# Performance work log

Hardware: AMD Instinct MI355X
Metric: run time of the kernel (lower is better)

Reference implementation:

```python
import jax, jax.numpy as jnp
import numpy as np

V_THRESH = 0.3

@jax.custom_vjp
def spike(x):
    return (x > 0).astype(x.dtype)

def _spike_fwd(x):
    return spike(x), x

def _spike_bwd(x, g):
    # rectangular straight-through surrogate gradient (pass grad where |x| < 0.5)
    return (g * (jnp.abs(x) < 0.5).astype(g.dtype),)

spike.defvjp(_spike_fwd, _spike_bwd)


def setup_inputs() -> dict:
    key = jax.random.key(0)
    B, T, H = 128, 2048, 128
    k1, = jax.random.split(key, 1)
    x_seq = jax.random.normal(k1, (B, T, H), dtype=jnp.float32)
    v0 = jnp.zeros((B, H), dtype=jnp.float32)
    z0 = jnp.zeros((B, H), dtype=jnp.float32)
    decay_raw = jnp.zeros((H,), dtype=jnp.float32)  # nn.initializers.constant(0.0)
    return {"x_seq": x_seq, "v0": v0, "z0": z0, "decay_raw": decay_raw}


def reference(x_seq, v0, z0, decay_raw):
    # LIF recurrence: v_t = v_{t-1} * decay * (1 - z_{t-1}) + x_t ; z_t = spike(v_t - v_thresh)
    decay = jax.nn.sigmoid(decay_raw)  # (H,)

    def step(carry, x_t):
        v, z = carry
        v = v * decay * (1.0 - z) + x_t
        z_out = spike(v - V_THRESH)
        return (v, z_out), z_out

    x_tb = jnp.swapaxes(x_seq, 0, 1)  # [T, B, H] for lax.scan over time
    (_, _), spk_tb = jax.lax.scan(step, (v0, z0), x_tb)
    return jnp.swapaxes(spk_tb, 0, 1)  # [B, T, H]
```

## Files before the change

### kernel.cpp

```cpp
#include <hip/hip_runtime.h>
#include <math.h>


constexpr int Bdim = 128;
constexpr int Tdim = 2048;
constexpr int Hdim = 128;
constexpr int HW   = 64;
constexpr int U    = 128;
constexpr int NBUF = 4;
constexpr int NW   = 8;
constexpr int NTILE = Tdim / U;
constexpr float VTH = 0.3f;

typedef const __attribute__((address_space(1))) void* gptr_t;
typedef __attribute__((address_space(3))) void* lptr_t;

__global__ __launch_bounds__(NW * 64) void lif_kernel(
    const float* __restrict__ x,
    const float* __restrict__ v0,
    const float* __restrict__ z0,
    const float* __restrict__ decay_raw,
    float* __restrict__ out)
{
    __shared__ float lds[NBUF][U][HW];

    const int tid  = threadIdx.x;
    const int wave = tid >> 6;
    const int lane = tid & 63;
    const int blk  = blockIdx.x;
    const int b    = blk >> 1;
    const int h0   = (blk & 1) * HW;

    const float* xbase = x   + (size_t)b * Tdim * Hdim + h0;
    float*       obase = out + (size_t)b * Tdim * Hdim + h0;

    const int sub = (lane >> 4) * Hdim + (lane & 15) * 4;

    auto fill = [&](int tile, int buf) {
        const float* g = xbase + (size_t)tile * U * Hdim + sub;
        #pragma unroll
        for (int q = 0; q < 4; ++q) {
            const int jj = wave * 4 + q;
            __builtin_amdgcn_global_load_lds(
                (gptr_t)(const void*)(g + (size_t)(4 * jj) * Hdim),
                (lptr_t)(void*)&lds[buf][4 * jj][0],
                16, 0, 0);
        }
    };

    auto flush = [&](int tile, int buf) {
        #pragma unroll
        for (int q = 0; q < 4; ++q) {
            const int s   = wave * 4 + q;
            const int row = 4 * s + (lane >> 4);
            const int col = (lane & 15) * 4;
            const float4 vv = *(const float4*)&lds[buf][row][col];
            *(float4*)(obase + (size_t)(tile * U + row) * Hdim + col) = vv;
        }
    };

    float decay = 0.f, v = 0.f, z = 0.f;
    if (wave == 0) {
        decay = 1.0f / (1.0f + expf(-decay_raw[h0 + lane]));
        v = v0[b * Hdim + h0 + lane];
        z = z0[b * Hdim + h0 + lane];
    }

    fill(0, 0);
    fill(1, 1);
    __syncthreads();

    for (int k = 0; k < NTILE; ++k) {
        if (k + 2 < NTILE) fill(k + 2, (k + 2) % NBUF);
        if (k >= 1)        flush(k - 1, (k - 1) % NBUF);

        if (wave == 0) {
            const int cb = k % NBUF;
            #pragma unroll 16
            for (int tl = 0; tl < U; ++tl) {
                const float xv = lds[cb][tl][lane];
                const float vd = v * decay;
                v = ((z > 0.5f) ? 0.0f : vd) + xv;
                z = (v > VTH) ? 1.0f : 0.0f;
                lds[cb][tl][lane] = z;
            }
        }
        __syncthreads();
    }
    flush(NTILE - 1, (NTILE - 1) % NBUF);
}

extern "C" void kernel_launch(void* const* d_in, const int* in_sizes, int n_in,
                              void* d_out, int out_size, void* d_ws, size_t ws_size,
                              hipStream_t stream) {
    const float* x         = (const float*)d_in[0];
    const float* v0        = (const float*)d_in[1];
    const float* z0        = (const float*)d_in[2];
    const float* decay_raw = (const float*)d_in[3];
    float* out = (float*)d_out;

    lif_kernel<<<Bdim * Hdim / HW, NW * 64, 0, stream>>>(x, v0, z0, decay_raw, out);
}
```

Before: 242.0 us.

## Specialize waves into compute, loader and storer roles with explicit waitcnt barriers

Moves from 8 waves to 4 per block with fixed roles. Wave 0 runs the recurrence and double-buffers its LDS reads of x in 16-step register batches. Waves 1-2 issue async global-to-LDS loads and wait on vmcnt counters instead of a full drain. Wave 3 flushes finished tiles to global memory. Raw s_barrier and waitcnt asm replace __syncthreads, which removes wasted work on the compute wave. The risk is correctness: the hand-tuned vmcnt thresholds and barrier placement must be right for the 4-buffer ring to be safe.

```diff
diff --git a/kernel.cpp b/kernel.cpp
--- a/kernel.cpp
+++ b/kernel.cpp
@@ -8,14 +8,18 @@
 constexpr int HW   = 64;
 constexpr int U    = 128;
 constexpr int NBUF = 4;
-constexpr int NW   = 8;
 constexpr int NTILE = Tdim / U;
 constexpr float VTH = 0.3f;
 
 typedef const __attribute__((address_space(1))) void* gptr_t;
 typedef __attribute__((address_space(3))) void* lptr_t;
 
-__global__ __launch_bounds__(NW * 64) void lif_kernel(
+#define BAR()     asm volatile("s_barrier" ::: "memory")
+#define WAITV16() asm volatile("s_waitcnt vmcnt(16)" ::: "memory")
+#define WAITV0()  asm volatile("s_waitcnt vmcnt(0)" ::: "memory")
+#define WAITL0()  asm volatile("s_waitcnt lgkmcnt(0)" ::: "memory")
+
+__global__ __launch_bounds__(256) void lif_kernel(
     const float* __restrict__ x,
     const float* __restrict__ v0,
     const float* __restrict__ z0,
@@ -39,8 +43,8 @@
     auto fill = [&](int tile, int buf) {
         const float* g = xbase + (size_t)tile * U * Hdim + sub;
         #pragma unroll
-        for (int q = 0; q < 4; ++q) {
-            const int jj = wave * 4 + q;
+        for (int q = 0; q < 16; ++q) {
+            const int jj = (wave - 1) * 16 + q;
             __builtin_amdgcn_global_load_lds(
                 (gptr_t)(const void*)(g + (size_t)(4 * jj) * Hdim),
                 (lptr_t)(void*)&lds[buf][4 * jj][0],
@@ -50,8 +54,7 @@
 
     auto flush = [&](int tile, int buf) {
         #pragma unroll
-        for (int q = 0; q < 4; ++q) {
-            const int s   = wave * 4 + q;
+        for (int s = 0; s < 32; ++s) {
             const int row = 4 * s + (lane >> 4);
             const int col = (lane & 15) * 4;
             const float4 vv = *(const float4*)&lds[buf][row][col];
@@ -64,30 +67,51 @@
         decay = 1.0f / (1.0f + expf(-decay_raw[h0 + lane]));
         v = v0[b * Hdim + h0 + lane];
         z = z0[b * Hdim + h0 + lane];
+    } else if (wave <= 2) {
+        fill(0, 0);
+        fill(1, 1);
+        WAITV16();
     }
-
-    fill(0, 0);
-    fill(1, 1);
-    __syncthreads();
+    BAR();
 
     for (int k = 0; k < NTILE; ++k) {
-        if (k + 2 < NTILE) fill(k + 2, (k + 2) % NBUF);
-        if (k >= 1)        flush(k - 1, (k - 1) % NBUF);
-
         if (wave == 0) {
-            const int cb = k % NBUF;
-            #pragma unroll 16
-            for (int tl = 0; tl < U; ++tl) {
-                const float xv = lds[cb][tl][lane];
-                const float vd = v * decay;
-                v = ((z > 0.5f) ? 0.0f : vd) + xv;
-                z = (v > VTH) ? 1.0f : 0.0f;
-                lds[cb][tl][lane] = z;
+            const int cb = k & 3;
+            float xa[16], xb[16];
+            #pragma unroll
+            for (int j = 0; j < 16; ++j) xa[j] = lds[cb][j][lane];
+            #pragma unroll
+            for (int g = 0; g < 8; ++g) {
+                if (g < 7) {
+                    #pragma unroll
+                    for (int j = 0; j < 16; ++j) {
+                        const float t = lds[cb][(g + 1) * 16 + j][lane];
+                        if (g & 1) xa[j] = t; else xb[j] = t;
+                    }
+                }
+                #pragma unroll
+                for (int j = 0; j < 16; ++j) {
+                    const float xv = (g & 1) ? xb[j] : xa[j];
+                    const float vd = v * decay;
+                    v = ((z > 0.5f) ? 0.0f : vd) + xv;
+                    z = (v > VTH) ? 1.0f : 0.0f;
+                    lds[cb][g * 16 + j][lane] = z;
+                }
             }
+            WAITL0();
+        } else if (wave <= 2) {
+            if (k + 2 < NTILE) {
+                fill(k + 2, (k + 2) & 3);
+                WAITV16();
+            } else {
+                WAITV0();
+            }
+        } else {
+            if (k >= 1) flush(k - 1, (k - 1) & 3);
         }
-        __syncthreads();
+        BAR();
     }
-    flush(NTILE - 1, (NTILE - 1) % NBUF);
+    if (wave == 3) flush(NTILE - 1, (NTILE - 1) & 3);
 }
 
 extern "C" void kernel_launch(void* const* d_in, const int* in_sizes, int n_in,
@@ -99,5 +123,5 @@
     const float* decay_raw = (const float*)d_in[3];
     float* out = (float*)d_out;
 
-    lif_kernel<<<Bdim * Hdim / HW, NW * 64, 0, stream>>>(x, v0, z0, decay_raw, out);
+    lif_kernel<<<Bdim * Hdim / HW, 256, 0, stream>>>(x, v0, z0, decay_raw, out);
 }
```

Result: slower. 247.0 us (+2.1%).

## Specialize waves into producer loaders and a compute wave writing spikes directly

Applied to the files above, without the earlier changes.

Splits the block into one compute wave and four loader waves. The loader waves prefetch x tiles three deep into LDS with explicit vmcnt waits and raw s_barrier. The compute wave register-double-buffers LDS reads in groups of eight and writes spikes straight to global memory, which removes the LDS write-back and separate flush pass. The aim is to shorten the serial recurrence's critical path and overlap loads with compute, at the cost of uncoalesced per-lane scalar global stores and hand-tuned barrier and waitcnt counts that must stay matched across the two roles.

```diff
diff --git a/kernel.cpp b/kernel.cpp
--- a/kernel.cpp
+++ b/kernel.cpp
@@ -7,13 +7,15 @@
 constexpr int Hdim = 128;
 constexpr int HW   = 64;
 constexpr int U    = 128;
-constexpr int NBUF = 4;
-constexpr int NW   = 8;
+constexpr int XBUF = 4;
 constexpr int NTILE = Tdim / U;
+constexpr int NW   = 5;
 constexpr float VTH = 0.3f;
 
 typedef const __attribute__((address_space(1))) void* gptr_t;
 typedef __attribute__((address_space(3))) void* lptr_t;
+
+#define BAR() asm volatile("s_barrier" ::: "memory")
 
 __global__ __launch_bounds__(NW * 64) void lif_kernel(
     const float* __restrict__ x,
@@ -22,7 +24,7 @@
     const float* __restrict__ decay_raw,
     float* __restrict__ out)
 {
-    __shared__ float lds[NBUF][U][HW];
+    __shared__ float xs[XBUF][U][HW];
 
     const int tid  = threadIdx.x;
     const int wave = tid >> 6;
@@ -34,60 +36,75 @@
     const float* xbase = x   + (size_t)b * Tdim * Hdim + h0;
     float*       obase = out + (size_t)b * Tdim * Hdim + h0;
 
-    const int sub = (lane >> 4) * Hdim + (lane & 15) * 4;
+    if (wave == 0) {
+        const float decay = 1.0f / (1.0f + expf(-decay_raw[h0 + lane]));
+        float v = v0[b * Hdim + h0 + lane];
+        float z = z0[b * Hdim + h0 + lane];
+        float* ol = obase + lane;
 
-    auto fill = [&](int tile, int buf) {
-        const float* g = xbase + (size_t)tile * U * Hdim + sub;
-        #pragma unroll
-        for (int q = 0; q < 4; ++q) {
-            const int jj = wave * 4 + q;
-            __builtin_amdgcn_global_load_lds(
-                (gptr_t)(const void*)(g + (size_t)(4 * jj) * Hdim),
-                (lptr_t)(void*)&lds[buf][4 * jj][0],
-                16, 0, 0);
+        BAR();
+
+        for (int k = 0; k < NTILE; ++k) {
+            const float (*xt)[HW] = xs[k & 3];
+            float xa[8], xb[8], zb[8];
+            #pragma unroll
+            for (int j = 0; j < 8; ++j) xa[j] = xt[j][lane];
+
+            #pragma unroll
+            for (int bt = 0; bt < 16; ++bt) {
+                if (bt < 15) {
+                    #pragma unroll
+                    for (int j = 0; j < 8; ++j) {
+                        const float t = xt[(bt + 1) * 8 + j][lane];
+                        if (bt & 1) xa[j] = t; else xb[j] = t;
+                    }
+                }
+                #pragma unroll
+                for (int j = 0; j < 8; ++j) {
+                    const float xv = (bt & 1) ? xb[j] : xa[j];
+                    const float vd = v * decay;
+                    v = ((z > 0.5f) ? 0.0f : vd) + xv;
+                    z = (v > VTH) ? 1.0f : 0.0f;
+                    zb[j] = z;
+                }
+                const size_t t0 = (size_t)k * U + bt * 8;
+                #pragma unroll
+                for (int j = 0; j < 8; ++j)
+                    ol[(t0 + j) * Hdim] = zb[j];
+            }
+            BAR();
         }
-    };
+    } else {
+        const int sub = (lane >> 4) * Hdim + (lane & 15) * 4;
 
-    auto flush = [&](int tile, int buf) {
-        #pragma unroll
-        for (int q = 0; q < 4; ++q) {
-            const int s   = wave * 4 + q;
-            const int row = 4 * s + (lane >> 4);
-            const int col = (lane & 15) * 4;
-            const float4 vv = *(const float4*)&lds[buf][row][col];
-            *(float4*)(obase + (size_t)(tile * U + row) * Hdim + col) = vv;
+        auto fill = [&](int tile, int buf) {
+            const float* g = xbase + (size_t)tile * U * Hdim + sub;
+            #pragma unroll
+            for (int q = 0; q < 8; ++q) {
+                const int jj = (wave - 1) * 8 + q;
+                __builtin_amdgcn_global_load_lds(
+                    (gptr_t)(const void*)(g + (size_t)(4 * jj) * Hdim),
+                    (lptr_t)(void*)&xs[buf][4 * jj][0],
+                    16, 0, 0);
+            }
+        };
+
+        fill(0, 0); fill(1, 1); fill(2, 2);
+        asm volatile("s_waitcnt vmcnt(16)" ::: "memory");
+        BAR();
+
+        for (int k = 0; k < NTILE; ++k) {
+            if (k + 3 < NTILE) {
+                fill(k + 3, (k + 3) & 3);
+                asm volatile("s_waitcnt vmcnt(16)" ::: "memory");
+            } else if (k == NTILE - 3) {
+                asm volatile("s_waitcnt vmcnt(8)" ::: "memory");
+            } else if (k == NTILE - 2) {
+                asm volatile("s_waitcnt vmcnt(0)" ::: "memory");
+            }
+            BAR();
         }
-    };
-
-    float decay = 0.f, v = 0.f, z = 0.f;
-    if (wave == 0) {
-        decay = 1.0f / (1.0f + expf(-decay_raw[h0 + lane]));
-        v = v0[b * Hdim + h0 + lane];
-        z = z0[b * Hdim + h0 + lane];
     }
-
-    fill(0, 0);
-    fill(1, 1);
-    __syncthreads();
-
-    for (int k = 0; k < NTILE; ++k) {
-        if (k + 2 < NTILE) fill(k + 2, (k + 2) % NBUF);
-        if (k >= 1)        flush(k - 1, (k - 1) % NBUF);
-
-        if (wave == 0) {
-            const int cb = k % NBUF;
-            #pragma unroll 16
-            for (int tl = 0; tl < U; ++tl) {
-                const float xv = lds[cb][tl][lane];
-                const float vd = v * decay;
-                v = ((z > 0.5f) ? 0.0f : vd) + xv;
-                z = (v > VTH) ? 1.0f : 0.0f;
-                lds[cb][tl][lane] = z;
-            }
-        }
-        __syncthreads();
-    }
-    flush(NTILE - 1, (NTILE - 1) % NBUF);
 }
 
 extern "C" void kernel_launch(void* const* d_in, const int* in_sizes, int n_in,
```

Measured after the change: 249.5 us. 1.03x slower.
